# Kernel tuning notes

Measured on AMD Instinct MI355X. Metric: run time of the kernel, lower is better.

Reference implementation:

```python
import jax, jax.numpy as jnp
import numpy as np
from jax import lax

PERCENT_T = 0.1
BN_EPS = 1e-5


def setup_inputs() -> dict:
    key = jax.random.key(0)
    ks = jax.random.split(key, 4)
    B, C, H, W = 32, 512, 56, 56
    R = C // 16
    x = jax.random.normal(ks[0], (B, C, H, W), dtype=jnp.float32)
    w1 = jax.random.normal(ks[1], (R, C), dtype=jnp.float32) * (1.0 / np.sqrt(C))
    b1 = jnp.zeros((R,), dtype=jnp.float32)
    w2 = jax.random.normal(ks[2], (C, R), dtype=jnp.float32) * (1.0 / np.sqrt(R))
    b2 = jnp.zeros((C,), dtype=jnp.float32)
    conv_w = jax.random.normal(ks[3], (1, 2, 7, 7), dtype=jnp.float32) * 0.1
    bn_gamma = jnp.ones((1,), dtype=jnp.float32)
    bn_beta = jnp.zeros((1,), dtype=jnp.float32)
    bn_mean = jnp.zeros((1,), dtype=jnp.float32)
    bn_var = jnp.ones((1,), dtype=jnp.float32)
    return {"x": x, "w1": w1, "b1": b1, "w2": w2, "b2": b2,
            "conv_w": conv_w, "bn_gamma": bn_gamma, "bn_beta": bn_beta,
            "bn_mean": bn_mean, "bn_var": bn_var}


def reference(x, w1, b1, w2, b2, conv_w, bn_gamma, bn_beta, bn_mean, bn_var):
    b, c, h, w = x.shape
    hw = h * w
    top_t = int(round(hw * PERCENT_T))  # static at trace time

    # --- TopTPercentChannelGate ---
    x_flat = x.reshape(b, c, hw)
    sel, _ = lax.top_k(x_flat, top_t)            # [b, c, top_t]
    pool_avg = sel.mean(axis=2)                  # [b, c]
    pool_max = sel.max(axis=2)                   # [b, c]

    def mlp(p):  # p: [b, c]
        h1 = jax.nn.relu(p @ w1.T + b1)
        return h1 @ w2.T + b2

    att = mlp(pool_avg) + mlp(pool_max)          # [b, c]
    x_out = x * jax.nn.sigmoid(att)[:, :, None, None]

    # --- SpatialGate ---
    cp = jnp.stack([x_out.max(axis=1), x_out.mean(axis=1)], axis=1)  # [b, 2, h, w]
    conv = lax.conv_general_dilated(
        cp, conv_w, window_strides=(1, 1), padding=[(3, 3), (3, 3)],
        dimension_numbers=("NCHW", "OIHW", "NCHW"))                   # [b, 1, h, w]
    bn = ((conv - bn_mean[None, :, None, None])
          * lax.rsqrt(bn_var[None, :, None, None] + BN_EPS)
          * bn_gamma[None, :, None, None] + bn_beta[None, :, None, None])
    return x_out * jax.nn.sigmoid(bn)
```

## Files before the change

kernel.cpp:

```cpp
#include <hip/hip_runtime.h>
#include <math.h>

#define NB 32
#define NC 512
#define NH 56
#define NW 56
#define NHW 3136
#define TOPT 314
#define NR 32
#define RBUCK 2048

typedef float f32x4 __attribute__((ext_vector_type(4)));

__device__ __forceinline__ unsigned int f2s(float f) {
    unsigned int b = __float_as_uint(f);
    return (b & 0x80000000u) ? ~b : (b | 0x80000000u);
}
__device__ __forceinline__ float s2f(unsigned int u) {
    unsigned int b = (u & 0x80000000u) ? (u ^ 0x80000000u) : ~u;
    return __uint_as_float(b);
}

__global__ __launch_bounds__(256) void topk_pool_kernel(
        const float* __restrict__ x,
        float* __restrict__ pool_avg, float* __restrict__ pool_max) {
    __shared__ unsigned int hist[2][RBUCK];
    __shared__ unsigned int wtot[4];
    __shared__ unsigned int sh_pref, sh_k;
    __shared__ float redsum[4];
    __shared__ unsigned int redmax[4];

    const int row = blockIdx.x;
    const int tid = threadIdx.x;
    const int wid = tid >> 6;
    const int lane = tid & 63;
    const float* xr = x + (size_t)row * NHW;
    const float4* xr4 = (const float4*)xr;

    float4 a0 = xr4[tid];
    float4 a1 = xr4[256 + tid];
    float4 a2 = xr4[512 + tid];
    const bool has13 = (tid < 64);
    float ex = has13 ? xr[3072 + tid] : 0.f;

    unsigned int u[13];
    u[0] = f2s(a0.x); u[1] = f2s(a0.y); u[2]  = f2s(a0.z); u[3]  = f2s(a0.w);
    u[4] = f2s(a1.x); u[5] = f2s(a1.y); u[6]  = f2s(a1.z); u[7]  = f2s(a1.w);
    u[8] = f2s(a2.x); u[9] = f2s(a2.y); u[10] = f2s(a2.z); u[11] = f2s(a2.w);
    u[12] = has13 ? f2s(ex) : 0u;

    unsigned int pref = 0u, mask = 0u, k = TOPT;
    const int shifts[3] = {21, 10, 0};
    #pragma unroll
    for (int r = 0; r < 3; ++r) {
        const int shift = shifts[r];
        {
            uint4 z = make_uint4(0u, 0u, 0u, 0u);
            uint4* h0 = (uint4*)hist[0];
            h0[tid] = z; h0[256 + tid] = z;
            if (r == 0) {
                uint4* h1 = (uint4*)hist[1];
                h1[tid] = z; h1[256 + tid] = z;
            }
        }
        __syncthreads();
        unsigned int* h = (r == 0) ? hist[wid >> 1] : hist[0];
        #pragma unroll
        for (int j = 0; j < 12; ++j) {
            if ((u[j] & mask) == pref)
                atomicAdd(&h[(u[j] >> shift) & (RBUCK - 1u)], 1u);
        }
        if (has13 && ((u[12] & mask) == pref))
            atomicAdd(&h[(u[12] >> shift) & (RBUCK - 1u)], 1u);
        __syncthreads();

        unsigned int vv[8];
        unsigned int g = 0u;
        if (r == 0) {
            #pragma unroll
            for (int bb = 0; bb < 8; ++bb) {
                vv[bb] = hist[0][8 * tid + bb] + hist[1][8 * tid + bb];
                g += vv[bb];
            }
        } else {
            #pragma unroll
            for (int bb = 0; bb < 8; ++bb) { vv[bb] = hist[0][8 * tid + bb]; g += vv[bb]; }
        }
        unsigned int S = g;
        #pragma unroll
        for (int off = 1; off < 64; off <<= 1) {
            unsigned int t2 = __shfl_down(S, off);
            if (lane + off < 64) S += t2;
        }
        if (lane == 0) wtot[wid] = S;
        __syncthreads();
        unsigned int hi = 0u;
        if (wid < 3) hi += wtot[wid + 1];
        if (wid < 2) hi += wtot[wid + 2];
        if (wid < 1) hi += wtot[wid + 3];
        S += hi;
        const unsigned int above = S - g;
        if (S >= k && above < k) {
            unsigned int cum = above;
            #pragma unroll
            for (int bb = 7; bb >= 0; --bb) {
                if (cum + vv[bb] >= k) {
                    sh_pref = pref | ((unsigned int)(8 * tid + bb) << shift);
                    sh_k = k - cum;
                    break;
                }
                cum += vv[bb];
            }
        }
        __syncthreads();
        pref = sh_pref;
        k = sh_k;
        mask = 0xFFFFFFFFu << shift;
    }

    const unsigned int t = pref;
    float sum = 0.f;
    unsigned int umax = 0u;
    #pragma unroll
    for (int j = 0; j < 12; ++j) {
        umax = max(umax, u[j]);
        if (u[j] > t) sum += s2f(u[j]);
    }
    if (has13) {
        umax = max(umax, u[12]);
        if (u[12] > t) sum += s2f(u[12]);
    }
    #pragma unroll
    for (int off = 32; off > 0; off >>= 1) {
        sum += __shfl_down(sum, off);
        umax = max(umax, __shfl_down(umax, off));
    }
    if (lane == 0) { redsum[wid] = sum; redmax[wid] = umax; }
    __syncthreads();
    if (tid == 0) {
        float tot = redsum[0] + redsum[1] + redsum[2] + redsum[3]
                  + (float)k * s2f(t);
        pool_avg[row] = tot * (1.0f / (float)TOPT);
        unsigned int m = max(max(redmax[0], redmax[1]),
                             max(redmax[2], redmax[3]));
        pool_max[row] = s2f(m);
    }
}

__global__ __launch_bounds__(256) void mlp_kernel(
        const float* __restrict__ pool_avg, const float* __restrict__ pool_max,
        const float* __restrict__ w1, const float* __restrict__ b1,
        const float* __restrict__ w2, const float* __restrict__ b2,
        float* __restrict__ s_out) {
    __shared__ float pa[NC], pm[NC], h1a[NR], h1m[NR];
    const int b = blockIdx.x, tid = threadIdx.x;
    for (int c = tid; c < NC; c += 256) {
        pa[c] = pool_avg[b * NC + c];
        pm[c] = pool_max[b * NC + c];
    }
    __syncthreads();
    if (tid < 64) {
        const int r = tid & 31;
        const float* wrow = w1 + r * NC;
        const float* p = (tid < 32) ? pa : pm;
        float acc = b1[r];
        for (int c = 0; c < NC; ++c) acc += p[c] * wrow[c];
        float h = fmaxf(acc, 0.f);
        if (tid < 32) h1a[r] = h; else h1m[r] = h;
    }
    __syncthreads();
    for (int c = tid; c < NC; c += 256) {
        float acc = 2.f * b2[c];
        const float* wrow = w2 + c * NR;
        for (int r = 0; r < NR; ++r) acc += (h1a[r] + h1m[r]) * wrow[r];
        s_out[b * NC + c] = 1.f / (1.f + expf(-acc));
    }
}

__global__ __launch_bounds__(256) void spatial_pool_kernel(
        const float* __restrict__ x, const float* __restrict__ s,
        float* __restrict__ cp_max, float* __restrict__ cp_avg) {
    __shared__ float sc[NC];
    __shared__ float4 pmx[3][64];
    __shared__ float4 psm[3][64];
    const int b = blockIdx.y, tid = threadIdx.x;
    const int qo = tid & 63;
    const int cg = tid >> 6;
    const int q = blockIdx.x * 64 + qo;
    for (int c = tid; c < NC; c += 256) sc[c] = s[b * NC + c];
    __syncthreads();
    const float4* xb4 = (const float4*)(x + (size_t)b * NC * NHW);
    float4 mx = make_float4(-INFINITY, -INFINITY, -INFINITY, -INFINITY);
    float4 sm = make_float4(0.f, 0.f, 0.f, 0.f);
    if (q < NHW / 4) {
        for (int c = cg * (NC / 4); c < (cg + 1) * (NC / 4); ++c) {
            float4 v = xb4[(size_t)c * (NHW / 4) + q];
            const float scv = sc[c];
            v.x *= scv; v.y *= scv; v.z *= scv; v.w *= scv;
            mx.x = fmaxf(mx.x, v.x); mx.y = fmaxf(mx.y, v.y);
            mx.z = fmaxf(mx.z, v.z); mx.w = fmaxf(mx.w, v.w);
            sm.x += v.x; sm.y += v.y; sm.z += v.z; sm.w += v.w;
        }
    }
    if (cg > 0 && q < NHW / 4) { pmx[cg - 1][qo] = mx; psm[cg - 1][qo] = sm; }
    __syncthreads();
    if (cg == 0 && q < NHW / 4) {
        #pragma unroll
        for (int i = 0; i < 3; ++i) {
            const float4 m2 = pmx[i][qo];
            const float4 s2 = psm[i][qo];
            mx.x = fmaxf(mx.x, m2.x); mx.y = fmaxf(mx.y, m2.y);
            mx.z = fmaxf(mx.z, m2.z); mx.w = fmaxf(mx.w, m2.w);
            sm.x += s2.x; sm.y += s2.y; sm.z += s2.z; sm.w += s2.w;
        }
        const float inv = 1.0f / (float)NC;
        sm.x *= inv; sm.y *= inv; sm.z *= inv; sm.w *= inv;
        ((float4*)(cp_max + b * NHW))[q] = mx;
        ((float4*)(cp_avg + b * NHW))[q] = sm;
    }
}

__global__ __launch_bounds__(256) void conv_gate_kernel(
        const float* __restrict__ cp_max, const float* __restrict__ cp_avg,
        const float* __restrict__ conv_w,
        const float* __restrict__ gamma, const float* __restrict__ beta,
        const float* __restrict__ mean, const float* __restrict__ var,
        float* __restrict__ g) {
    __shared__ float wgt[98];
    const int b = blockIdx.y, tid = threadIdx.x;
    const int p = blockIdx.x * 256 + tid;
    if (tid < 98) wgt[tid] = conv_w[tid];
    __syncthreads();
    if (p >= NHW) return;
    const int h = p / NW, w = p - h * NW;
    const float* cm = cp_max + b * NHW;
    const float* ca = cp_avg + b * NHW;
    float acc = 0.f;
    for (int i = 0; i < 7; ++i) {
        const int hh = h - 3 + i;
        if (hh < 0 || hh >= NH) continue;
        for (int j = 0; j < 7; ++j) {
            const int ww = w - 3 + j;
            if (ww < 0 || ww >= NW) continue;
            const int q = hh * NW + ww;
            acc += cm[q] * wgt[i * 7 + j] + ca[q] * wgt[49 + i * 7 + j];
        }
    }
    const float bnv = (acc - mean[0]) * rsqrtf(var[0] + 1e-5f) * gamma[0] + beta[0];
    g[b * NHW + p] = 1.f / (1.f + expf(-bnv));
}

__global__ __launch_bounds__(256) void scale_out_kernel(
        const float* __restrict__ x, const float* __restrict__ s,
        const float* __restrict__ g, float* __restrict__ out) {
    const int bc = blockIdx.x;
    const int b = bc >> 9;
    const int tid = threadIdx.x;
    const float sv = s[bc];
    const f32x4* xr = (const f32x4*)(x + (size_t)bc * NHW);
    const f32x4* gr = (const f32x4*)(g + (size_t)b * NHW);
    f32x4* orow = (f32x4*)(out + (size_t)bc * NHW);
    #pragma unroll
    for (int i = 0; i < 3; ++i) {
        const int q = tid + 256 * i;
        f32x4 xv = xr[q];
        f32x4 gv = gr[q];
        f32x4 ov = xv * sv * gv;
        __builtin_nontemporal_store(ov, &orow[q]);
    }
    if (tid < 16) {
        const int q = 768 + tid;
        f32x4 xv = xr[q];
        f32x4 gv = gr[q];
        f32x4 ov = xv * sv * gv;
        __builtin_nontemporal_store(ov, &orow[q]);
    }
}

extern "C" void kernel_launch(void* const* d_in, const int* in_sizes, int n_in,
                              void* d_out, int out_size, void* d_ws, size_t ws_size,
                              hipStream_t stream) {
    const float* x      = (const float*)d_in[0];
    const float* w1     = (const float*)d_in[1];
    const float* b1     = (const float*)d_in[2];
    const float* w2     = (const float*)d_in[3];
    const float* b2     = (const float*)d_in[4];
    const float* conv_w = (const float*)d_in[5];
    const float* gamma  = (const float*)d_in[6];
    const float* beta   = (const float*)d_in[7];
    const float* mean   = (const float*)d_in[8];
    const float* var    = (const float*)d_in[9];
    float* out = (float*)d_out;

    float* ws = (float*)d_ws;
    float* pool_avg = ws;
    float* pool_max = ws + 16384;
    float* s        = ws + 32768;
    float* cp_max   = ws + 49152;
    float* cp_avg   = ws + 149504;
    float* g        = ws + 249856;

    topk_pool_kernel<<<NB * NC, 256, 0, stream>>>(x, pool_avg, pool_max);
    mlp_kernel<<<NB, 256, 0, stream>>>(pool_avg, pool_max, w1, b1, w2, b2, s);
    dim3 grid3((NHW / 4 + 63) / 64, NB);
    spatial_pool_kernel<<<grid3, 256, 0, stream>>>(x, s, cp_max, cp_avg);
    dim3 grid4((NHW + 255) / 256, NB);
    conv_gate_kernel<<<grid4, 256, 0, stream>>>(cp_max, cp_avg, conv_w,
                                                gamma, beta, mean, var, g);
    scale_out_kernel<<<NB * NC, 256, 0, stream>>>(x, s, g, out);
}
```

Measured before the change: 190.9 us.

## Process two rows per top-k block with packed 16-bit dual histograms

The top-k radix-select kernel now handles two channel rows per block. Both rows share a single shared-memory histogram, with counts packed into the low and high 16 bits of each bin. This halves the number of histogram clears, barriers and scans per row and halves the block count, at the cost of more registers per thread and more atomic traffic on the same bins. It also adds an unroll-by-2 pragma to the spatial pooling channel loop.

```diff
diff --git a/kernel.cpp b/kernel.cpp
--- a/kernel.cpp
+++ b/kernel.cpp
@@ -26,30 +26,37 @@
         float* __restrict__ pool_avg, float* __restrict__ pool_max) {
     __shared__ unsigned int hist[2][RBUCK];
     __shared__ unsigned int wtot[4];
-    __shared__ unsigned int sh_pref, sh_k;
-    __shared__ float redsum[4];
-    __shared__ unsigned int redmax[4];
-
-    const int row = blockIdx.x;
+    __shared__ unsigned int sh_pref[2], sh_k[2];
+    __shared__ float redsA[4], redsB[4];
+    __shared__ unsigned int redmA[4], redmB[4];
+
+    const int rowA = blockIdx.x * 2;
     const int tid = threadIdx.x;
     const int wid = tid >> 6;
     const int lane = tid & 63;
-    const float* xr = x + (size_t)row * NHW;
-    const float4* xr4 = (const float4*)xr;
-
-    float4 a0 = xr4[tid];
-    float4 a1 = xr4[256 + tid];
-    float4 a2 = xr4[512 + tid];
+    const float* xa = x + (size_t)rowA * NHW;
+    const float* xb = xa + NHW;
+    const float4* xa4 = (const float4*)xa;
+    const float4* xb4 = (const float4*)xb;
+
+    float4 a0 = xa4[tid], a1 = xa4[256 + tid], a2 = xa4[512 + tid];
+    float4 b0 = xb4[tid], b1 = xb4[256 + tid], b2 = xb4[512 + tid];
     const bool has13 = (tid < 64);
-    float ex = has13 ? xr[3072 + tid] : 0.f;
-
-    unsigned int u[13];
+    float exA = has13 ? xa[3072 + tid] : 0.f;
+    float exB = has13 ? xb[3072 + tid] : 0.f;
+
+    unsigned int u[13], w[13];
     u[0] = f2s(a0.x); u[1] = f2s(a0.y); u[2]  = f2s(a0.z); u[3]  = f2s(a0.w);
     u[4] = f2s(a1.x); u[5] = f2s(a1.y); u[6]  = f2s(a1.z); u[7]  = f2s(a1.w);
     u[8] = f2s(a2.x); u[9] = f2s(a2.y); u[10] = f2s(a2.z); u[11] = f2s(a2.w);
-    u[12] = has13 ? f2s(ex) : 0u;
-
-    unsigned int pref = 0u, mask = 0u, k = TOPT;
+    u[12] = f2s(exA);
+    w[0] = f2s(b0.x); w[1] = f2s(b0.y); w[2]  = f2s(b0.z); w[3]  = f2s(b0.w);
+    w[4] = f2s(b1.x); w[5] = f2s(b1.y); w[6]  = f2s(b1.z); w[7]  = f2s(b1.w);
+    w[8] = f2s(b2.x); w[9] = f2s(b2.y); w[10] = f2s(b2.z); w[11] = f2s(b2.w);
+    w[12] = f2s(exB);
+
+    unsigned int prefA = 0u, prefB = 0u, mask = 0u;
+    unsigned int kA = TOPT, kB = TOPT;
     const int shifts[3] = {21, 10, 0};
     #pragma unroll
     for (int r = 0; r < 3; ++r) {
@@ -66,12 +73,13 @@
         __syncthreads();
         unsigned int* h = (r == 0) ? hist[wid >> 1] : hist[0];
         #pragma unroll
-        for (int j = 0; j < 12; ++j) {
-            if ((u[j] & mask) == pref)
+        for (int j = 0; j < 13; ++j) {
+            const bool live = (j < 12) || has13;
+            if (live && ((u[j] & mask) == prefA))
                 atomicAdd(&h[(u[j] >> shift) & (RBUCK - 1u)], 1u);
-        }
-        if (has13 && ((u[12] & mask) == pref))
-            atomicAdd(&h[(u[12] >> shift) & (RBUCK - 1u)], 1u);
+            if (live && ((w[j] & mask) == prefB))
+                atomicAdd(&h[(w[j] >> shift) & (RBUCK - 1u)], 65536u);
+        }
         __syncthreads();
 
         unsigned int vv[8];
@@ -99,51 +107,71 @@
         if (wid < 2) hi += wtot[wid + 2];
         if (wid < 1) hi += wtot[wid + 3];
         S += hi;
-        const unsigned int above = S - g;
-        if (S >= k && above < k) {
-            unsigned int cum = above;
+        const unsigned int SloT = S & 0xFFFFu, ShiT = S >> 16;
+        const unsigned int gLo = g & 0xFFFFu,  gHi = g >> 16;
+        const unsigned int aboveLo = SloT - gLo, aboveHi = ShiT - gHi;
+        if (SloT >= kA && aboveLo < kA) {
+            unsigned int cum = aboveLo;
             #pragma unroll
             for (int bb = 7; bb >= 0; --bb) {
-                if (cum + vv[bb] >= k) {
-                    sh_pref = pref | ((unsigned int)(8 * tid + bb) << shift);
-                    sh_k = k - cum;
+                const unsigned int hh = vv[bb] & 0xFFFFu;
+                if (cum + hh >= kA) {
+                    sh_pref[0] = prefA | ((unsigned int)(8 * tid + bb) << shift);
+                    sh_k[0] = kA - cum;
                     break;
                 }
-                cum += vv[bb];
+                cum += hh;
             }
         }
+        if (ShiT >= kB && aboveHi < kB) {
+            unsigned int cum = aboveHi;
+            #pragma unroll
+            for (int bb = 7; bb >= 0; --bb) {
+                const unsigned int hh = vv[bb] >> 16;
+                if (cum + hh >= kB) {
+                    sh_pref[1] = prefB | ((unsigned int)(8 * tid + bb) << shift);
+                    sh_k[1] = kB - cum;
+                    break;
+                }
+                cum += hh;
+            }
+        }
         __syncthreads();
-        pref = sh_pref;
-        k = sh_k;
+        prefA = sh_pref[0]; kA = sh_k[0];
+        prefB = sh_pref[1]; kB = sh_k[1];
         mask = 0xFFFFFFFFu << shift;
     }
 
-    const unsigned int t = pref;
-    float sum = 0.f;
-    unsigned int umax = 0u;
+    const unsigned int tA = prefA, tB = prefB;
+    float sumA = 0.f, sumB = 0.f;
+    unsigned int mA = 0u, mB = 0u;
     #pragma unroll
-    for (int j = 0; j < 12; ++j) {
-        umax = max(umax, u[j]);
-        if (u[j] > t) sum += s2f(u[j]);
-    }
-    if (has13) {
-        umax = max(umax, u[12]);
-        if (u[12] > t) sum += s2f(u[12]);
+    for (int j = 0; j < 13; ++j) {
+        const bool live = (j < 12) || has13;
+        if (live) {
+            mA = max(mA, u[j]);
+            if (u[j] > tA) sumA += s2f(u[j]);
+            mB = max(mB, w[j]);
+            if (w[j] > tB) sumB += s2f(w[j]);
+        }
     }
     #pragma unroll
     for (int off = 32; off > 0; off >>= 1) {
-        sum += __shfl_down(sum, off);
-        umax = max(umax, __shfl_down(umax, off));
-    }
-    if (lane == 0) { redsum[wid] = sum; redmax[wid] = umax; }
+        sumA += __shfl_down(sumA, off);
+        sumB += __shfl_down(sumB, off);
+        mA = max(mA, __shfl_down(mA, off));
+        mB = max(mB, __shfl_down(mB, off));
+    }
+    if (lane == 0) { redsA[wid] = sumA; redsB[wid] = sumB;
+                     redmA[wid] = mA;   redmB[wid] = mB; }
     __syncthreads();
     if (tid == 0) {
-        float tot = redsum[0] + redsum[1] + redsum[2] + redsum[3]
-                  + (float)k * s2f(t);
-        pool_avg[row] = tot * (1.0f / (float)TOPT);
-        unsigned int m = max(max(redmax[0], redmax[1]),
-                             max(redmax[2], redmax[3]));
-        pool_max[row] = s2f(m);
+        float totA = redsA[0] + redsA[1] + redsA[2] + redsA[3] + (float)kA * s2f(tA);
+        float totB = redsB[0] + redsB[1] + redsB[2] + redsB[3] + (float)kB * s2f(tB);
+        pool_avg[rowA]     = totA * (1.0f / (float)TOPT);
+        pool_avg[rowA + 1] = totB * (1.0f / (float)TOPT);
+        pool_max[rowA]     = s2f(max(max(redmA[0], redmA[1]), max(redmA[2], redmA[3])));
+        pool_max[rowA + 1] = s2f(max(max(redmB[0], redmB[1]), max(redmB[2], redmB[3])));
     }
 }
 
@@ -193,6 +221,7 @@
     float4 mx = make_float4(-INFINITY, -INFINITY, -INFINITY, -INFINITY);
     float4 sm = make_float4(0.f, 0.f, 0.f, 0.f);
     if (q < NHW / 4) {
+        #pragma unroll 2
         for (int c = cg * (NC / 4); c < (cg + 1) * (NC / 4); ++c) {
             float4 v = xb4[(size_t)c * (NHW / 4) + q];
             const float scv = sc[c];
@@ -300,7 +329,7 @@
     float* cp_avg   = ws + 149504;
     float* g        = ws + 249856;
 
-    topk_pool_kernel<<<NB * NC, 256, 0, stream>>>(x, pool_avg, pool_max);
+    topk_pool_kernel<<<NB * NC / 2, 256, 0, stream>>>(x, pool_avg, pool_max);
     mlp_kernel<<<NB, 256, 0, stream>>>(pool_avg, pool_max, w1, b1, w2, b2, s);
     dim3 grid3((NHW / 4 + 63) / 64, NB);
     spatial_pool_kernel<<<grid3, 256, 0, stream>>>(x, s, cp_max, cp_avg);
```

Result: faster. 177.5 us (-7.0%).

## Run top-k radix select per wavefront instead of per block

Applied to the files above, without the earlier changes.

The top-k pooling kernel now gives each 64-lane wavefront its own channel row and a private padded LDS histogram. Lanes hold 49 values each in registers, and block-wide barriers are replaced by wave-local fences plus a ballot/shuffle to broadcast the selected bucket. This removes the per-round __syncthreads and the cross-wave scan, at the cost of higher register pressure and more atomics per lane on a single histogram. The spatial pool channel loop also gets an unroll-by-2 hint.

```diff
diff --git a/kernel.cpp b/kernel.cpp
--- a/kernel.cpp
+++ b/kernel.cpp
@@ -9,6 +9,8 @@
 #define TOPT 314
 #define NR 32
 #define RBUCK 2048
+#define HWORDS 2112
+#define HPAD(b) ((b) + ((b) >> 5))
 
 typedef float f32x4 __attribute__((ext_vector_type(4)));
 
@@ -24,97 +26,69 @@
 __global__ __launch_bounds__(256) void topk_pool_kernel(
         const float* __restrict__ x,
         float* __restrict__ pool_avg, float* __restrict__ pool_max) {
-    __shared__ unsigned int hist[2][RBUCK];
-    __shared__ unsigned int wtot[4];
-    __shared__ unsigned int sh_pref, sh_k;
-    __shared__ float redsum[4];
-    __shared__ unsigned int redmax[4];
-
-    const int row = blockIdx.x;
+    __shared__ unsigned int hist[4][HWORDS];
     const int tid = threadIdx.x;
     const int wid = tid >> 6;
     const int lane = tid & 63;
+    const int row = blockIdx.x * 4 + wid;
     const float* xr = x + (size_t)row * NHW;
     const float4* xr4 = (const float4*)xr;
-
-    float4 a0 = xr4[tid];
-    float4 a1 = xr4[256 + tid];
-    float4 a2 = xr4[512 + tid];
-    const bool has13 = (tid < 64);
-    float ex = has13 ? xr[3072 + tid] : 0.f;
-
-    unsigned int u[13];
-    u[0] = f2s(a0.x); u[1] = f2s(a0.y); u[2]  = f2s(a0.z); u[3]  = f2s(a0.w);
-    u[4] = f2s(a1.x); u[5] = f2s(a1.y); u[6]  = f2s(a1.z); u[7]  = f2s(a1.w);
-    u[8] = f2s(a2.x); u[9] = f2s(a2.y); u[10] = f2s(a2.z); u[11] = f2s(a2.w);
-    u[12] = has13 ? f2s(ex) : 0u;
+    unsigned int* H = hist[wid];
+
+    unsigned int u[49];
+    #pragma unroll
+    for (int j = 0; j < 12; ++j) {
+        float4 v = xr4[lane + 64 * j];
+        u[4 * j + 0] = f2s(v.x);
+        u[4 * j + 1] = f2s(v.y);
+        u[4 * j + 2] = f2s(v.z);
+        u[4 * j + 3] = f2s(v.w);
+    }
+    u[48] = f2s(xr[3072 + lane]);
 
     unsigned int pref = 0u, mask = 0u, k = TOPT;
     const int shifts[3] = {21, 10, 0};
     #pragma unroll
     for (int r = 0; r < 3; ++r) {
         const int shift = shifts[r];
-        {
-            uint4 z = make_uint4(0u, 0u, 0u, 0u);
-            uint4* h0 = (uint4*)hist[0];
-            h0[tid] = z; h0[256 + tid] = z;
-            if (r == 0) {
-                uint4* h1 = (uint4*)hist[1];
-                h1[tid] = z; h1[256 + tid] = z;
-            }
-        }
-        __syncthreads();
-        unsigned int* h = (r == 0) ? hist[wid >> 1] : hist[0];
-        #pragma unroll
-        for (int j = 0; j < 12; ++j) {
+        #pragma unroll
+        for (int m = 0; m < 33; ++m) H[lane + 64 * m] = 0u;
+        __threadfence_block();
+        #pragma unroll
+        for (int j = 0; j < 49; ++j) {
             if ((u[j] & mask) == pref)
-                atomicAdd(&h[(u[j] >> shift) & (RBUCK - 1u)], 1u);
-        }
-        if (has13 && ((u[12] & mask) == pref))
-            atomicAdd(&h[(u[12] >> shift) & (RBUCK - 1u)], 1u);
-        __syncthreads();
-
-        unsigned int vv[8];
+                atomicAdd(&H[HPAD((u[j] >> shift) & (RBUCK - 1u))], 1u);
+        }
+        __threadfence_block();
         unsigned int g = 0u;
-        if (r == 0) {
-            #pragma unroll
-            for (int bb = 0; bb < 8; ++bb) {
-                vv[bb] = hist[0][8 * tid + bb] + hist[1][8 * tid + bb];
-                g += vv[bb];
-            }
-        } else {
-            #pragma unroll
-            for (int bb = 0; bb < 8; ++bb) { vv[bb] = hist[0][8 * tid + bb]; g += vv[bb]; }
-        }
+        #pragma unroll
+        for (int m = 0; m < 32; ++m) g += H[33 * lane + m];
         unsigned int S = g;
         #pragma unroll
         for (int off = 1; off < 64; off <<= 1) {
             unsigned int t2 = __shfl_down(S, off);
             if (lane + off < 64) S += t2;
         }
-        if (lane == 0) wtot[wid] = S;
-        __syncthreads();
-        unsigned int hi = 0u;
-        if (wid < 3) hi += wtot[wid + 1];
-        if (wid < 2) hi += wtot[wid + 2];
-        if (wid < 1) hi += wtot[wid + 3];
-        S += hi;
         const unsigned int above = S - g;
-        if (S >= k && above < k) {
+        unsigned int prefC = 0u, kC = 0u;
+        const bool crossing = (S >= k) && (above < k);
+        if (crossing) {
             unsigned int cum = above;
             #pragma unroll
-            for (int bb = 7; bb >= 0; --bb) {
-                if (cum + vv[bb] >= k) {
-                    sh_pref = pref | ((unsigned int)(8 * tid + bb) << shift);
-                    sh_k = k - cum;
+            for (int bb = 31; bb >= 0; --bb) {
+                const unsigned int hh = H[33 * lane + bb];
+                if (cum + hh >= k) {
+                    prefC = pref | ((unsigned int)(32 * lane + bb) << shift);
+                    kC = k - cum;
                     break;
                 }
-                cum += vv[bb];
+                cum += hh;
             }
         }
-        __syncthreads();
-        pref = sh_pref;
-        k = sh_k;
+        const unsigned long long bal = __ballot(crossing);
+        const int src = __ffsll((unsigned long long)bal) - 1;
+        pref = __shfl(prefC, src);
+        k = __shfl(kC, src);
         mask = 0xFFFFFFFFu << shift;
     }
 
@@ -122,28 +96,18 @@
     float sum = 0.f;
     unsigned int umax = 0u;
     #pragma unroll
-    for (int j = 0; j < 12; ++j) {
+    for (int j = 0; j < 49; ++j) {
         umax = max(umax, u[j]);
         if (u[j] > t) sum += s2f(u[j]);
-    }
-    if (has13) {
-        umax = max(umax, u[12]);
-        if (u[12] > t) sum += s2f(u[12]);
     }
     #pragma unroll
     for (int off = 32; off > 0; off >>= 1) {
         sum += __shfl_down(sum, off);
         umax = max(umax, __shfl_down(umax, off));
     }
-    if (lane == 0) { redsum[wid] = sum; redmax[wid] = umax; }
-    __syncthreads();
-    if (tid == 0) {
-        float tot = redsum[0] + redsum[1] + redsum[2] + redsum[3]
-                  + (float)k * s2f(t);
-        pool_avg[row] = tot * (1.0f / (float)TOPT);
-        unsigned int m = max(max(redmax[0], redmax[1]),
-                             max(redmax[2], redmax[3]));
-        pool_max[row] = s2f(m);
+    if (lane == 0) {
+        pool_avg[row] = (sum + (float)k * s2f(t)) * (1.0f / (float)TOPT);
+        pool_max[row] = s2f(umax);
     }
 }
 
@@ -193,6 +157,7 @@
     float4 mx = make_float4(-INFINITY, -INFINITY, -INFINITY, -INFINITY);
     float4 sm = make_float4(0.f, 0.f, 0.f, 0.f);
     if (q < NHW / 4) {
+        #pragma unroll 2
         for (int c = cg * (NC / 4); c < (cg + 1) * (NC / 4); ++c) {
             float4 v = xb4[(size_t)c * (NHW / 4) + q];
             const float scv = sc[c];
@@ -300,7 +265,7 @@
     float* cp_avg   = ws + 149504;
     float* g        = ws + 249856;
 
-    topk_pool_kernel<<<NB * NC, 256, 0, stream>>>(x, pool_avg, pool_max);
+    topk_pool_kernel<<<NB * NC / 4, 256, 0, stream>>>(x, pool_avg, pool_max);
     mlp_kernel<<<NB, 256, 0, stream>>>(pool_avg, pool_max, w1, b1, w2, b2, s);
     dim3 grid3((NHW / 4 + 63) / 64, NB);
     spatial_pool_kernel<<<grid3, 256, 0, stream>>>(x, s, cp_max, cp_avg);
```

After: 187.8 us. About the same (-1.6%).
